# Kernel tuning notes

Measured on AMD Instinct MI355X. Metric: run time of the kernel, lower is better.

The kernel has to match this reference:

```python
import jax, jax.numpy as jnp
import numpy as np

VOCAB = 32000
EMB = 512       # embedding_size; also the sequence length per the source loop
HID = 512       # hidden_dim
NTAG = 36       # number of POS-tag-specific LSTMCells
OUT = 1         # output_size
SEQ = EMB       # forward iterates range(embedding_size)


def setup_inputs() -> dict:
    key = jax.random.key(0)
    ks = jax.random.split(key, 10)
    s = 1.0 / np.sqrt(HID)  # torch LSTMCell init: U(-1/sqrt(H), 1/sqrt(H))
    inp = {
        "x": jax.random.randint(ks[0], (1, SEQ), 0, VOCAB, dtype=jnp.int64)
             if jax.config.jax_enable_x64 else
             jax.random.randint(ks[0], (1, SEQ), 0, VOCAB, dtype=jnp.int32),
        "tag_ids": jax.random.randint(ks[1], (SEQ,), 0, NTAG, dtype=jnp.int32),
        "h0": jnp.zeros((1, HID), jnp.float32),
        "c0": jnp.zeros((1, HID), jnp.float32),
        # frozen pretrained embedding table
        "emb": jax.random.normal(ks[2], (VOCAB, EMB), jnp.float32) * 0.1,
        # stacked per-tag LSTMCell params, torch gate order (i, f, g, o)
        "W_ih": jax.random.uniform(ks[3], (NTAG, 4 * HID, EMB), jnp.float32, -s, s),
        "W_hh": jax.random.uniform(ks[4], (NTAG, 4 * HID, HID), jnp.float32, -s, s),
        "b_ih": jax.random.uniform(ks[5], (NTAG, 4 * HID), jnp.float32, -s, s),
        "b_hh": jax.random.uniform(ks[6], (NTAG, 4 * HID), jnp.float32, -s, s),
        "W_fc": jax.random.uniform(ks[7], (OUT, HID), jnp.float32, -s, s),
        "b_fc": jax.random.uniform(ks[8], (OUT,), jnp.float32, -s, s),
    }
    return inp


def _lstm_cell(x_t, h, c, Wih, Whh, bih, bhh):
    # x_t: [D], h/c: [H]; Wih: [4H, D], Whh: [4H, H]
    gates = Wih @ x_t + Whh @ h + bih + bhh      # [4H]
    i, f, g, o = jnp.split(gates, 4)
    i, f, o = jax.nn.sigmoid(i), jax.nn.sigmoid(f), jax.nn.sigmoid(o)
    g = jnp.tanh(g)
    c_new = f * c + i * g
    h_new = o * jnp.tanh(c_new)
    return h_new, c_new


def reference(x, tag_ids, h0, c0, emb, W_ih, W_hh, b_ih, b_hh, W_fc, b_fc):
    embeds = emb[x[0]]                            # [T, D] (batch is structurally 1)

    def step(carry, xs):
        h, c = carry
        x_t, tag = xs
        h, c = _lstm_cell(x_t, h, c, W_ih[tag], W_hh[tag], b_ih[tag], b_hh[tag])
        return (h, c), None

    (h, c), _ = jax.lax.scan(step, (h0[0], c0[0]), (embeds, tag_ids))
    # dropout is identity in eval; fc + sigmoid; out[:, -1]
    out = jax.nn.sigmoid(h @ W_fc.T + b_fc)       # [OUT]
    out = out.reshape(1, -1)[:, -1]               # [1]
    return out, h[None, :], c[None, :]
```

## Files before the change

### kernel.cpp

```cpp
#include <hip/hip_runtime.h>

#define VOCAB 32000
#define EMB 512
#define HID 512
#define NTAG 36
#define SEQ 512
#define G4H 2048
#define NBLK 128
#define XCHUNK 32

typedef unsigned long long ull;

__device__ __forceinline__ float fast_tanh(float x) {
    float e = __expf(2.f * x);
    return 1.f - 2.f / (e + 1.f);
}
__device__ __forceinline__ float fast_sigmoid(float x) {
    return 1.f / (1.f + __expf(-x));
}

__global__ __launch_bounds__(256) void precompute_z(
    const int* __restrict__ x,
    const int* __restrict__ tag_ids,
    const float* __restrict__ emb,
    const float* __restrict__ W_ih,
    const float* __restrict__ b_ih,
    const float* __restrict__ b_hh,
    float* __restrict__ Z)
{
    __shared__ int list[SEQ];
    __shared__ int cnt;
    __shared__ __align__(16) float xc[XCHUNK][EMB];

    const int tid  = threadIdx.x;
    const int tag  = blockIdx.x;
    const int row0 = blockIdx.y * 64;
    const int wave = tid >> 6, lane = tid & 63;

    if (tid == 0) cnt = 0;
    __syncthreads();
    for (int t = tid; t < SEQ; t += 256)
        if (tag_ids[t] == tag) { int p = atomicAdd(&cnt, 1); list[p] = t; }
    __syncthreads();
    const int n = cnt;

    for (int c0 = 0; c0 < n; c0 += XCHUNK) {
        const int nc = min(XCHUNK, n - c0);
        __syncthreads();
        for (int idx = tid; idx < nc * 128; idx += 256) {
            int tl = idx >> 7, k4 = idx & 127;
            int t = list[c0 + tl];
            ((float4*)xc[tl])[k4] = ((const float4*)(emb + (size_t)x[t] * EMB))[k4];
        }
        __syncthreads();
        for (int rr = 0; rr < 16; rr += 4) {
            const int row = row0 + wave * 16 + rr;
            const float* w0p = W_ih + ((size_t)tag * G4H + row) * EMB;
            const float* w1p = w0p + EMB;
            const float* w2p = w0p + 2 * EMB;
            const float* w3p = w0p + 3 * EMB;
            const float4 wa0 = ((const float4*)w0p)[lane], wa1 = ((const float4*)w0p)[64 + lane];
            const float4 wb0 = ((const float4*)w1p)[lane], wb1 = ((const float4*)w1p)[64 + lane];
            const float4 wc0 = ((const float4*)w2p)[lane], wc1 = ((const float4*)w2p)[64 + lane];
            const float4 wd0 = ((const float4*)w3p)[lane], wd1 = ((const float4*)w3p)[64 + lane];
            const float bi0 = b_ih[tag * G4H + row]     + b_hh[tag * G4H + row];
            const float bi1 = b_ih[tag * G4H + row + 1] + b_hh[tag * G4H + row + 1];
            const float bi2 = b_ih[tag * G4H + row + 2] + b_hh[tag * G4H + row + 2];
            const float bi3 = b_ih[tag * G4H + row + 3] + b_hh[tag * G4H + row + 3];
            for (int tl = 0; tl < nc; ++tl) {
                float4 x0 = *(const float4*)&xc[tl][4 * lane];
                float4 x1 = *(const float4*)&xc[tl][256 + 4 * lane];
                float d0 = wa0.x*x0.x + wa0.y*x0.y + wa0.z*x0.z + wa0.w*x0.w
                         + wa1.x*x1.x + wa1.y*x1.y + wa1.z*x1.z + wa1.w*x1.w;
                float d1 = wb0.x*x0.x + wb0.y*x0.y + wb0.z*x0.z + wb0.w*x0.w
                         + wb1.x*x1.x + wb1.y*x1.y + wb1.z*x1.z + wb1.w*x1.w;
                float d2 = wc0.x*x0.x + wc0.y*x0.y + wc0.z*x0.z + wc0.w*x0.w
                         + wc1.x*x1.x + wc1.y*x1.y + wc1.z*x1.z + wc1.w*x1.w;
                float d3 = wd0.x*x0.x + wd0.y*x0.y + wd0.z*x0.z + wd0.w*x0.w
                         + wd1.x*x1.x + wd1.y*x1.y + wd1.z*x1.z + wd1.w*x1.w;
                #pragma unroll
                for (int m = 32; m >= 1; m >>= 1) {
                    d0 += __shfl_xor(d0, m, 64);
                    d1 += __shfl_xor(d1, m, 64);
                    d2 += __shfl_xor(d2, m, 64);
                    d3 += __shfl_xor(d3, m, 64);
                }
                if (lane == 0) {
                    float* zr = Z + (size_t)list[c0 + tl] * G4H + row;
                    zr[0] = d0 + bi0; zr[1] = d1 + bi1;
                    zr[2] = d2 + bi2; zr[3] = d3 + bi3;
                }
            }
        }
    }
}

__global__ __launch_bounds__(256) void lstm_seq(
    const int* __restrict__ tag_ids,
    const float* __restrict__ h0,
    const float* __restrict__ c0,
    const float* __restrict__ W_hh,
    const float* __restrict__ Z,
    const float* __restrict__ W_fc,
    const float* __restrict__ b_fc,
    ull* __restrict__ hist,
    float* __restrict__ d_out)
{
    __shared__ int tags[SEQ];
    __shared__ __align__(16) float hsh[2][HID];
    __shared__ float red[256];

    const int tid  = threadIdx.x;
    const int b    = blockIdx.x;
    const int wave = tid >> 6, lane = tid & 63;
    const int j    = b * 4 + wave;

    for (int t = tid; t < SEQ; t += 256) tags[t] = tag_ids[t];
    __syncthreads();

    float c    = (lane == 0) ? c0[j] : 0.f;
    float hval = 0.f;

    for (int t = 0; t < SEQ; ++t) {
        const int tag = tags[t];
        const float* wbase = W_hh + (size_t)tag * G4H * HID;
        const float4* r;
        r = (const float4*)(wbase + (size_t)(j)        * HID);
        float4 wi0 = r[lane], wi1 = r[64 + lane];
        r = (const float4*)(wbase + (size_t)(512 + j)  * HID);
        float4 wf0 = r[lane], wf1 = r[64 + lane];
        r = (const float4*)(wbase + (size_t)(1024 + j) * HID);
        float4 wg0 = r[lane], wg1 = r[64 + lane];
        r = (const float4*)(wbase + (size_t)(1536 + j) * HID);
        float4 wo0 = r[lane], wo1 = r[64 + lane];

        float zi = 0.f, zf = 0.f, zg = 0.f, zo = 0.f;
        if (lane == 0) {
            const float* zt = Z + (size_t)t * G4H;
            zi = zt[j]; zf = zt[512 + j]; zg = zt[1024 + j]; zo = zt[1536 + j];
        }

        asm volatile("s_waitcnt vmcnt(0)" ::: "memory");

        float v0, v1;
        if (t == 0) {
            v0 = h0[2 * tid]; v1 = h0[2 * tid + 1];
        } else {
            const ull* pa = hist + (size_t)(t - 1) * HID + 2 * tid;
            const ull* pb = pa + 1;
            const unsigned want = (unsigned)t;
            ull a0 = __hip_atomic_load(pa, __ATOMIC_RELAXED, __HIP_MEMORY_SCOPE_AGENT);
            ull b0 = __hip_atomic_load(pb, __ATOMIC_RELAXED, __HIP_MEMORY_SCOPE_AGENT);
            ull a1 = __hip_atomic_load(pa, __ATOMIC_RELAXED, __HIP_MEMORY_SCOPE_AGENT);
            ull b1 = __hip_atomic_load(pb, __ATOMIC_RELAXED, __HIP_MEMORY_SCOPE_AGENT);
            ull a2 = __hip_atomic_load(pa, __ATOMIC_RELAXED, __HIP_MEMORY_SCOPE_AGENT);
            ull b2 = __hip_atomic_load(pb, __ATOMIC_RELAXED, __HIP_MEMORY_SCOPE_AGENT);
            while ((unsigned)(a0 >> 32) != want || (unsigned)(b0 >> 32) != want) {
                a0 = a1; b0 = b1;
                a1 = a2; b1 = b2;
                a2 = __hip_atomic_load(pa, __ATOMIC_RELAXED, __HIP_MEMORY_SCOPE_AGENT);
                b2 = __hip_atomic_load(pb, __ATOMIC_RELAXED, __HIP_MEMORY_SCOPE_AGENT);
            }
            v0 = __uint_as_float((unsigned)a0);
            v1 = __uint_as_float((unsigned)b0);
        }
        const int hb = t & 1;
        hsh[hb][2 * tid]     = v0;
        hsh[hb][2 * tid + 1] = v1;
        __syncthreads();

        const float4 ha = *(const float4*)&hsh[hb][4 * lane];
        const float4 hc = *(const float4*)&hsh[hb][256 + 4 * lane];

        float di = wi0.x*ha.x + wi0.y*ha.y + wi0.z*ha.z + wi0.w*ha.w
                 + wi1.x*hc.x + wi1.y*hc.y + wi1.z*hc.z + wi1.w*hc.w;
        float df = wf0.x*ha.x + wf0.y*ha.y + wf0.z*ha.z + wf0.w*ha.w
                 + wf1.x*hc.x + wf1.y*hc.y + wf1.z*hc.z + wf1.w*hc.w;
        float dg = wg0.x*ha.x + wg0.y*ha.y + wg0.z*ha.z + wg0.w*ha.w
                 + wg1.x*hc.x + wg1.y*hc.y + wg1.z*hc.z + wg1.w*hc.w;
        float do_ = wo0.x*ha.x + wo0.y*ha.y + wo0.z*ha.z + wo0.w*ha.w
                  + wo1.x*hc.x + wo1.y*hc.y + wo1.z*hc.z + wo1.w*hc.w;
        #pragma unroll
        for (int m = 32; m >= 1; m >>= 1) {
            di  += __shfl_xor(di,  m, 64);
            df  += __shfl_xor(df,  m, 64);
            dg  += __shfl_xor(dg,  m, 64);
            do_ += __shfl_xor(do_, m, 64);
        }

        if (lane == 0) {
            float gi = zi + di, gf = zf + df, gg = zg + dg, go = zo + do_;
            float si = fast_sigmoid(gi);
            float sf = fast_sigmoid(gf);
            float so = fast_sigmoid(go);
            float tg = fast_tanh(gg);
            c = sf * c + si * tg;
            hval = so * fast_tanh(c);
            ull pk = ((ull)(unsigned)(t + 1) << 32) | (ull)__float_as_uint(hval);
            __hip_atomic_store(&hist[(size_t)t * HID + j], pk,
                               __ATOMIC_RELAXED, __HIP_MEMORY_SCOPE_AGENT);
        }
    }

    if (lane == 0) {
        d_out[1 + j]       = hval;
        d_out[1 + HID + j] = c;
    }

    if (b == 0) {
        const ull* hp = hist + (size_t)(SEQ - 1) * HID;
        ull a  = __hip_atomic_load(&hp[2 * tid],     __ATOMIC_RELAXED, __HIP_MEMORY_SCOPE_AGENT);
        ull bq = __hip_atomic_load(&hp[2 * tid + 1], __ATOMIC_RELAXED, __HIP_MEMORY_SCOPE_AGENT);
        while ((unsigned)(a >> 32) != (unsigned)SEQ || (unsigned)(bq >> 32) != (unsigned)SEQ) {
            a  = __hip_atomic_load(&hp[2 * tid],     __ATOMIC_RELAXED, __HIP_MEMORY_SCOPE_AGENT);
            bq = __hip_atomic_load(&hp[2 * tid + 1], __ATOMIC_RELAXED, __HIP_MEMORY_SCOPE_AGENT);
        }
        float s = __uint_as_float((unsigned)a)  * W_fc[2 * tid]
                + __uint_as_float((unsigned)bq) * W_fc[2 * tid + 1];
        red[tid] = s;
        __syncthreads();
        #pragma unroll
        for (int off = 128; off > 0; off >>= 1) {
            if (tid < off) red[tid] += red[tid + off];
            __syncthreads();
        }
        if (tid == 0)
            d_out[0] = fast_sigmoid(red[0] + b_fc[0]);
    }
}

extern "C" void kernel_launch(void* const* d_in, const int* in_sizes, int n_in,
                              void* d_out, int out_size, void* d_ws, size_t ws_size,
                              hipStream_t stream) {
    const int*   x       = (const int*)d_in[0];
    const int*   tag_ids = (const int*)d_in[1];
    const float* h0      = (const float*)d_in[2];
    const float* c0      = (const float*)d_in[3];
    const float* emb     = (const float*)d_in[4];
    const float* W_ih    = (const float*)d_in[5];
    const float* W_hh    = (const float*)d_in[6];
    const float* b_ih    = (const float*)d_in[7];
    const float* b_hh    = (const float*)d_in[8];
    const float* W_fc    = (const float*)d_in[9];
    const float* b_fc    = (const float*)d_in[10];
    float* out = (float*)d_out;

    const size_t zBytes = (size_t)SEQ * G4H * sizeof(float);
    float* Z    = (float*)d_ws;
    ull*   hist = (ull*)((char*)d_ws + zBytes);

    dim3 gA(NTAG, 32);
    precompute_z<<<gA, 256, 0, stream>>>(x, tag_ids, emb, W_ih, b_ih, b_hh, Z);
    lstm_seq<<<NBLK, 256, 0, stream>>>(tag_ids, h0, c0, W_hh, Z, W_fc, b_fc,
                                       hist, out);
}
```

Measured before the change: 1.329 ms.

## Replace per-element hist polling with per-block step counters polled by one wave

Each block now publishes a padded per-block step counter after its four h values are stored. Only wave 0 polls the 128 counters, then reads the 512 h values with tag validation. This replaces the old scheme where all 256 threads spun directly on tagged hist entries, and it drops the explicit vmcnt wait and the double-buffered shared h. The aim is to cut polling traffic to the hist cache lines. In exchange each step gains an extra __syncthreads, a counter store, and a memset launch.

```diff
diff --git a/kernel.cpp b/kernel.cpp
--- a/kernel.cpp
+++ b/kernel.cpp
@@ -10,6 +10,9 @@
 #define XCHUNK 32
 
 typedef unsigned long long ull;
+
+#define RLX __ATOMIC_RELAXED
+#define AGT __HIP_MEMORY_SCOPE_AGENT
 
 __device__ __forceinline__ float fast_tanh(float x) {
     float e = __expf(2.f * x);
@@ -104,10 +107,11 @@
     const float* __restrict__ W_fc,
     const float* __restrict__ b_fc,
     ull* __restrict__ hist,
+    ull* __restrict__ cnt,
     float* __restrict__ d_out)
 {
     __shared__ int tags[SEQ];
-    __shared__ __align__(16) float hsh[2][HID];
+    __shared__ __align__(16) float hsh[HID];
     __shared__ float red[256];
 
     const int tid  = threadIdx.x;
@@ -118,7 +122,7 @@
     for (int t = tid; t < SEQ; t += 256) tags[t] = tag_ids[t];
     __syncthreads();
 
-    float c    = (lane == 0) ? c0[j] : 0.f;
+    float cc   = (lane == 0) ? c0[j] : 0.f;
     float hval = 0.f;
 
     for (int t = 0; t < SEQ; ++t) {
@@ -140,37 +144,49 @@
             zi = zt[j]; zf = zt[512 + j]; zg = zt[1024 + j]; zo = zt[1536 + j];
         }
 
-        asm volatile("s_waitcnt vmcnt(0)" ::: "memory");
-
-        float v0, v1;
         if (t == 0) {
-            v0 = h0[2 * tid]; v1 = h0[2 * tid + 1];
-        } else {
-            const ull* pa = hist + (size_t)(t - 1) * HID + 2 * tid;
-            const ull* pb = pa + 1;
-            const unsigned want = (unsigned)t;
-            ull a0 = __hip_atomic_load(pa, __ATOMIC_RELAXED, __HIP_MEMORY_SCOPE_AGENT);
-            ull b0 = __hip_atomic_load(pb, __ATOMIC_RELAXED, __HIP_MEMORY_SCOPE_AGENT);
-            ull a1 = __hip_atomic_load(pa, __ATOMIC_RELAXED, __HIP_MEMORY_SCOPE_AGENT);
-            ull b1 = __hip_atomic_load(pb, __ATOMIC_RELAXED, __HIP_MEMORY_SCOPE_AGENT);
-            ull a2 = __hip_atomic_load(pa, __ATOMIC_RELAXED, __HIP_MEMORY_SCOPE_AGENT);
-            ull b2 = __hip_atomic_load(pb, __ATOMIC_RELAXED, __HIP_MEMORY_SCOPE_AGENT);
-            while ((unsigned)(a0 >> 32) != want || (unsigned)(b0 >> 32) != want) {
-                a0 = a1; b0 = b1;
-                a1 = a2; b1 = b2;
-                a2 = __hip_atomic_load(pa, __ATOMIC_RELAXED, __HIP_MEMORY_SCOPE_AGENT);
-                b2 = __hip_atomic_load(pb, __ATOMIC_RELAXED, __HIP_MEMORY_SCOPE_AGENT);
-            }
-            v0 = __uint_as_float((unsigned)a0);
-            v1 = __uint_as_float((unsigned)b0);
-        }
-        const int hb = t & 1;
-        hsh[hb][2 * tid]     = v0;
-        hsh[hb][2 * tid + 1] = v1;
-        __syncthreads();
-
-        const float4 ha = *(const float4*)&hsh[hb][4 * lane];
-        const float4 hc = *(const float4*)&hsh[hb][256 + 4 * lane];
+            if (wave == 0) {
+                float4 a = ((const float4*)h0)[2 * lane];
+                float4 d = ((const float4*)h0)[2 * lane + 1];
+                ((float4*)hsh)[2 * lane]     = a;
+                ((float4*)hsh)[2 * lane + 1] = d;
+            }
+        } else if (wave == 0) {
+            const ull want = (ull)t;
+            ull ca = __hip_atomic_load(&cnt[(2 * lane)     * 8], RLX, AGT);
+            ull cb = __hip_atomic_load(&cnt[(2 * lane + 1) * 8], RLX, AGT);
+            while (!__all(ca >= want && cb >= want)) {
+                ca = __hip_atomic_load(&cnt[(2 * lane)     * 8], RLX, AGT);
+                cb = __hip_atomic_load(&cnt[(2 * lane + 1) * 8], RLX, AGT);
+            }
+            const ull* hp = hist + (size_t)(t - 1) * HID + 8 * lane;
+            ull v[8];
+            for (;;) {
+                #pragma unroll
+                for (int q = 0; q < 8; ++q)
+                    v[q] = __hip_atomic_load(&hp[q], RLX, AGT);
+                bool good = true;
+                #pragma unroll
+                for (int q = 0; q < 8; ++q)
+                    good = good && ((unsigned)(v[q] >> 32) == (unsigned)t);
+                if (__all(good)) break;
+            }
+            float4 f0, f1;
+            f0.x = __uint_as_float((unsigned)v[0]);
+            f0.y = __uint_as_float((unsigned)v[1]);
+            f0.z = __uint_as_float((unsigned)v[2]);
+            f0.w = __uint_as_float((unsigned)v[3]);
+            f1.x = __uint_as_float((unsigned)v[4]);
+            f1.y = __uint_as_float((unsigned)v[5]);
+            f1.z = __uint_as_float((unsigned)v[6]);
+            f1.w = __uint_as_float((unsigned)v[7]);
+            ((float4*)hsh)[2 * lane]     = f0;
+            ((float4*)hsh)[2 * lane + 1] = f1;
+        }
+        __syncthreads();
+
+        const float4 ha = *(const float4*)&hsh[4 * lane];
+        const float4 hc = *(const float4*)&hsh[256 + 4 * lane];
 
         float di = wi0.x*ha.x + wi0.y*ha.y + wi0.z*ha.z + wi0.w*ha.w
                  + wi1.x*hc.x + wi1.y*hc.y + wi1.z*hc.z + wi1.w*hc.w;
@@ -194,29 +210,48 @@
             float sf = fast_sigmoid(gf);
             float so = fast_sigmoid(go);
             float tg = fast_tanh(gg);
-            c = sf * c + si * tg;
-            hval = so * fast_tanh(c);
+            cc   = sf * cc + si * tg;
+            hval = so * fast_tanh(cc);
             ull pk = ((ull)(unsigned)(t + 1) << 32) | (ull)__float_as_uint(hval);
-            __hip_atomic_store(&hist[(size_t)t * HID + j], pk,
-                               __ATOMIC_RELAXED, __HIP_MEMORY_SCOPE_AGENT);
-        }
+            __hip_atomic_store(&hist[(size_t)t * HID + j], pk, RLX, AGT);
+        }
+        __syncthreads();
+        if (tid == 0)
+            __hip_atomic_store(&cnt[b * 8], (ull)(unsigned)(t + 1), RLX, AGT);
     }
 
     if (lane == 0) {
         d_out[1 + j]       = hval;
-        d_out[1 + HID + j] = c;
+        d_out[1 + HID + j] = cc;
     }
 
     if (b == 0) {
-        const ull* hp = hist + (size_t)(SEQ - 1) * HID;
-        ull a  = __hip_atomic_load(&hp[2 * tid],     __ATOMIC_RELAXED, __HIP_MEMORY_SCOPE_AGENT);
-        ull bq = __hip_atomic_load(&hp[2 * tid + 1], __ATOMIC_RELAXED, __HIP_MEMORY_SCOPE_AGENT);
-        while ((unsigned)(a >> 32) != (unsigned)SEQ || (unsigned)(bq >> 32) != (unsigned)SEQ) {
-            a  = __hip_atomic_load(&hp[2 * tid],     __ATOMIC_RELAXED, __HIP_MEMORY_SCOPE_AGENT);
-            bq = __hip_atomic_load(&hp[2 * tid + 1], __ATOMIC_RELAXED, __HIP_MEMORY_SCOPE_AGENT);
-        }
-        float s = __uint_as_float((unsigned)a)  * W_fc[2 * tid]
-                + __uint_as_float((unsigned)bq) * W_fc[2 * tid + 1];
+        if (wave == 0) {
+            const ull want = (ull)SEQ;
+            ull ca = __hip_atomic_load(&cnt[(2 * lane)     * 8], RLX, AGT);
+            ull cb = __hip_atomic_load(&cnt[(2 * lane + 1) * 8], RLX, AGT);
+            while (!__all(ca >= want && cb >= want)) {
+                ca = __hip_atomic_load(&cnt[(2 * lane)     * 8], RLX, AGT);
+                cb = __hip_atomic_load(&cnt[(2 * lane + 1) * 8], RLX, AGT);
+            }
+            const ull* hp = hist + (size_t)(SEQ - 1) * HID + 8 * lane;
+            ull v[8];
+            for (;;) {
+                #pragma unroll
+                for (int q = 0; q < 8; ++q)
+                    v[q] = __hip_atomic_load(&hp[q], RLX, AGT);
+                bool good = true;
+                #pragma unroll
+                for (int q = 0; q < 8; ++q)
+                    good = good && ((unsigned)(v[q] >> 32) == (unsigned)SEQ);
+                if (__all(good)) break;
+            }
+            #pragma unroll
+            for (int q = 0; q < 8; ++q)
+                hsh[8 * lane + q] = __uint_as_float((unsigned)v[q]);
+        }
+        __syncthreads();
+        float s = hsh[2 * tid] * W_fc[2 * tid] + hsh[2 * tid + 1] * W_fc[2 * tid + 1];
         red[tid] = s;
         __syncthreads();
         #pragma unroll
@@ -246,11 +281,15 @@
     float* out = (float*)d_out;
 
     const size_t zBytes = (size_t)SEQ * G4H * sizeof(float);
+    const size_t hBytes = (size_t)SEQ * HID * sizeof(ull);
     float* Z    = (float*)d_ws;
     ull*   hist = (ull*)((char*)d_ws + zBytes);
+    ull*   cnt  = (ull*)((char*)d_ws + zBytes + hBytes);
+
+    hipMemsetAsync(cnt, 0, NBLK * 8 * sizeof(ull), stream);
 
     dim3 gA(NTAG, 32);
     precompute_z<<<gA, 256, 0, stream>>>(x, tag_ids, emb, W_ih, b_ih, b_hh, Z);
     lstm_seq<<<NBLK, 256, 0, stream>>>(tag_ids, h0, c0, W_hh, Z, W_fc, b_fc,
-                                       hist, out);
-}
+                                       hist, cnt, out);
+}
```

Result: slower. 1.501 ms (+13.0%).
